# Kernel tuning notes

Hardware: AMD Instinct MI355X
Metric: run time of the kernel (lower is better)

The kernel has to match this reference:

```python
import jax, jax.numpy as jnp
import numpy as np

B, S, D = 2, 2048, 1024
H = 16
HD = D // H  # 64


def setup_inputs() -> dict:
    key = jax.random.key(0)
    k = jax.random.split(key, 6)
    s = 0.02
    return {
        "x": jax.random.normal(k[0], (B, S, D), dtype=jnp.float32),
        "wq": jax.random.normal(k[1], (D, D), dtype=jnp.float32) * s,
        "wk": jax.random.normal(k[2], (D, D), dtype=jnp.float32) * s,
        "wv": jax.random.normal(k[3], (D, D), dtype=jnp.float32) * s,
        "wo": jax.random.normal(k[4], (D, D), dtype=jnp.float32) * s,
        "bo": jnp.zeros((D,), dtype=jnp.float32),
    }


def reference(x, wq, wk, wv, wo, bo):
    b, n, d = x.shape
    # nn.Linear: y = x @ W.T (qkv_bias=False)
    def proj(w):
        y = jnp.einsum('bnd,od->bno', x, w)
        return y.reshape(b, n, H, HD).transpose(0, 2, 1, 3)  # (b, H, n, hd)
    q, k, v = proj(wq), proj(wk), proj(wv)
    scores = jnp.einsum('bhqd,bhkd->bhqk', q, k) / jnp.sqrt(jnp.float32(HD))
    # NOTE: source code slices the causal mask but never applies it; softmax is unmasked.
    attn = jax.nn.softmax(scores, axis=-1)
    # dropout p=0.0 -> identity
    ctx = jnp.einsum('bhqk,bhkd->bhqd', attn, v)
    ctx = ctx.transpose(0, 2, 1, 3).reshape(b, n, d)
    return jnp.einsum('bnd,od->bno', ctx, wo) + bo
```

## Files before the change

kernel.cpp:

```cpp
#include <hip/hip_runtime.h>
#include <hip/hip_bf16.h>
#include <stdint.h>

typedef __attribute__((ext_vector_type(8))) short short8;
typedef __attribute__((ext_vector_type(4))) float float4v;
typedef __attribute__((ext_vector_type(4))) unsigned short ushort4v;

#define Bq 2
#define Sq 2048
#define Dq 1024
#define Hq 16
#define HDq 64

#define QSCALE 0.18033688011112042f

__device__ __forceinline__ unsigned short f2bf(float f) {
  union { float f; uint32_t u; } v; v.f = f;
  uint32_t r = (v.u + 0x7FFFu + ((v.u >> 16) & 1u)) >> 16;
  return (unsigned short)r;
}

__device__ __forceinline__ uint32_t pk2bf(float a, float b) {
  union { __hip_bfloat162 h; uint32_t u; } cv;
  cv.h = __float22bfloat162_rn(make_float2(a, b));
  return cv.u;
}

__device__ __forceinline__ void gl_lds16(const unsigned short* g, unsigned short* l) {
  __builtin_amdgcn_global_load_lds(
      (const __attribute__((address_space(1))) void*)g,
      (__attribute__((address_space(3))) void*)l, 16, 0, 0);
}

__global__ __launch_bounds__(256) void cvt_all_kernel(
    const float* __restrict__ x,
    const float* __restrict__ w0, const float* __restrict__ w1,
    const float* __restrict__ w2, const float* __restrict__ w3,
    unsigned short* __restrict__ xb, unsigned short* __restrict__ wb) {
  const int bid = blockIdx.x;
  const float* src;
  unsigned short* dst;
  int idx;
  if (bid < 4096) {
    src = x; dst = xb;
    idx = bid * 256 + threadIdx.x;
  } else {
    int j = (bid - 4096) * 256 + threadIdx.x;
    int z = j >> 18;
    src = (z == 0) ? w0 : (z == 1) ? w1 : (z == 2) ? w2 : w3;
    dst = wb + (size_t)z * 1048576;
    idx = j & 262143;
  }
  float4v f = ((const float4v*)src)[idx];
  ushort4v o;
#pragma unroll
  for (int q = 0; q < 4; q++) o[q] = f2bf(f[q]);
  ((ushort4v*)dst)[idx] = o;
}

template <bool OUTPROJ, int MT>
__global__ __launch_bounds__(256) void gemm_bt_kernel(
    const unsigned short* __restrict__ A,
    const unsigned short* __restrict__ W0,
    const unsigned short* __restrict__ W1,
    const unsigned short* __restrict__ W2,
    unsigned short* __restrict__ q_dst,
    unsigned short* __restrict__ k_dst,
    unsigned short* __restrict__ v_dst,
    float* __restrict__ f_dst,
    const float* __restrict__ bias) {
  constexpr int K = 1024;
  constexpr int NMB = MT / 32;
  constexpr int APASS = MT / 32;
  const int z = blockIdx.z;
  const unsigned short* W = (z == 0) ? W0 : (z == 1) ? W1 : W2;
  unsigned short* qkv = (z == 0) ? q_dst : (z == 1) ? k_dst : v_dst;

  __shared__ unsigned short Asm[MT * 64];
  __shared__ unsigned short Bsm[128 * 64];

  const int t = threadIdx.x;
  const int wave = t >> 6, lane = t & 63;
  const int quad = lane >> 4, l16 = lane & 15;
  const int wy = wave >> 1, wx = wave & 1;
  const int row0 = blockIdx.x * MT;
  const int col0 = blockIdx.y * 128;

  float4v zero = {0.f, 0.f, 0.f, 0.f};
  float4v acc[NMB][4];
#pragma unroll
  for (int i = 0; i < NMB; i++)
#pragma unroll
    for (int j = 0; j < 4; j++) acc[i][j] = zero;

  const int srow = t >> 3;
  const int sgl = ((t & 7) ^ (srow & 7)) << 3;
  const unsigned short* gA[APASS];
  const unsigned short* gB[4];
#pragma unroll
  for (int i = 0; i < APASS; i++)
    gA[i] = A + (size_t)(row0 + i * 32 + srow) * K + sgl;
#pragma unroll
  for (int i = 0; i < 4; i++)
    gB[i] = W + (size_t)(col0 + i * 32 + srow) * K + sgl;

  const int swl = (l16 & 7);

  for (int k0 = 0; k0 < K; k0 += 64) {
#pragma unroll
    for (int i = 0; i < APASS; i++) gl_lds16(gA[i] + k0, &Asm[i * 2048 + t * 8]);
#pragma unroll
    for (int i = 0; i < 4; i++) gl_lds16(gB[i] + k0, &Bsm[i * 2048 + t * 8]);
    __syncthreads();
    short8 af[NMB][2], bf[4][2];
#pragma unroll
    for (int ks = 0; ks < 2; ks++) {
#pragma unroll
      for (int mb = 0; mb < NMB; mb++) {
        int row = wy * (MT / 2) + mb * 16 + l16;
        int pg = (ks * 4 + quad) ^ swl;
        af[mb][ks] = *(const short8*)(&Asm[row * 64 + pg * 8]);
      }
#pragma unroll
      for (int nb = 0; nb < 4; nb++) {
        int row = wx * 64 + nb * 16 + l16;
        int pg = (ks * 4 + quad) ^ swl;
        bf[nb][ks] = *(const short8*)(&Bsm[row * 64 + pg * 8]);
      }
    }
#pragma unroll
    for (int ks = 0; ks < 2; ks++)
#pragma unroll
      for (int mb = 0; mb < NMB; mb++)
#pragma unroll
        for (int nb = 0; nb < 4; nb++)
          acc[mb][nb] = __builtin_amdgcn_mfma_f32_16x16x32_bf16(af[mb][ks], bf[nb][ks], acc[mb][nb], 0, 0, 0);
    __syncthreads();
  }

  const float qsc = (!OUTPROJ && z == 0) ? QSCALE : 1.0f;
#pragma unroll
  for (int mb = 0; mb < NMB; mb++) {
#pragma unroll
    for (int nb = 0; nb < 4; nb++) {
#pragma unroll
      for (int r = 0; r < 4; r++) {
        int row = row0 + wy * (MT / 2) + mb * 16 + quad * 4 + r;
        int o = col0 + wx * 64 + nb * 16 + l16;
        float val = acc[mb][nb][r];
        if (OUTPROJ) {
          f_dst[(size_t)row * 1024 + o] = val + bias[o];
        } else {
          int b = row >> 11, s = row & 2047;
          int h = o >> 6, hd = o & 63;
          qkv[(size_t)((b * Hq + h) * Sq + s) * HDq + hd] = f2bf(val * qsc);
        }
      }
    }
  }
}

__global__ __launch_bounds__(256) void attn_kernel(
    const unsigned short* __restrict__ Q,
    const unsigned short* __restrict__ Kg,
    const unsigned short* __restrict__ Vg,
    unsigned short* __restrict__ ctx) {
  constexpr int KSTR = 68;
  constexpr int VSTR = 136;
  const int bh = blockIdx.y;
  const int q0 = blockIdx.x * 128;
  const int t = threadIdx.x;
  const int wave = t >> 6, lane = t & 63;
  const int quad = lane >> 4, l16 = lane & 15;

  __shared__ unsigned short Ksm[128 * KSTR];
  __shared__ unsigned short Vsm[64 * VSTR];

  const unsigned short* Qb = Q + (size_t)bh * Sq * HDq;
  const unsigned short* Kb = Kg + (size_t)bh * Sq * HDq;
  const unsigned short* Vb = Vg + (size_t)bh * Sq * HDq;

  short8 qf[2][2];
#pragma unroll
  for (int rb = 0; rb < 2; rb++)
#pragma unroll
    for (int ks = 0; ks < 2; ks++)
      qf[rb][ks] = *(const short8*)(Qb + (size_t)(q0 + wave * 32 + rb * 16 + l16) * HDq + ks * 32 + quad * 8);

  short8 ones;
#pragma unroll
  for (int j = 0; j < 8; j++) ones[j] = (short)0x3F80;

  float4v zero = {0.f, 0.f, 0.f, 0.f};
  float4v of[2][4];
  float4v dsum[2] = {zero, zero};
#pragma unroll
  for (int rb = 0; rb < 2; rb++)
#pragma unroll
    for (int hb = 0; hb < 4; hb++) of[rb][hb] = zero;

  const int kr0 = t >> 3, kc = (t & 7) << 3;
  const int vr2 = (t & 63) * 2;
  const int vc8 = (t >> 6) << 3;
  const int sig = (vr2 & ~31) + (((vr2 >> 2) & 3) << 3) + (((vr2 >> 4) & 1) << 2) + (vr2 & 3);

  short8 kpr[4], vpr0[2], vpr1[2];
#pragma unroll
  for (int i = 0; i < 4; i++)
    kpr[i] = *(const short8*)(Kb + (size_t)(kr0 + i * 32) * HDq + kc);
#pragma unroll
  for (int i = 0; i < 2; i++) {
    vpr0[i] = *(const short8*)(Vb + (size_t)vr2 * HDq + vc8 + i * 32);
    vpr1[i] = *(const short8*)(Vb + (size_t)(vr2 + 1) * HDq + vc8 + i * 32);
  }

  for (int kt = 0; kt < Sq; kt += 128) {
#pragma unroll
    for (int i = 0; i < 4; i++)
      *(short8*)(&Ksm[(kr0 + i * 32) * KSTR + kc]) = kpr[i];
#pragma unroll
    for (int i = 0; i < 2; i++)
#pragma unroll
      for (int j = 0; j < 8; j++) {
        uint32_t pk = (uint32_t)(unsigned short)vpr0[i][j] |
                      ((uint32_t)(unsigned short)vpr1[i][j] << 16);
        *(uint32_t*)(&Vsm[(vc8 + i * 32 + j) * VSTR + sig]) = pk;
      }
    __syncthreads();

    if (kt + 128 < Sq) {
      const unsigned short* Kn = Kb + (size_t)(kt + 128) * HDq;
      const unsigned short* Vn = Vb + (size_t)(kt + 128) * HDq;
#pragma unroll
      for (int i = 0; i < 4; i++)
        kpr[i] = *(const short8*)(Kn + (size_t)(kr0 + i * 32) * HDq + kc);
#pragma unroll
      for (int i = 0; i < 2; i++) {
        vpr0[i] = *(const short8*)(Vn + (size_t)vr2 * HDq + vc8 + i * 32);
        vpr1[i] = *(const short8*)(Vn + (size_t)(vr2 + 1) * HDq + vc8 + i * 32);
      }
    }

#pragma unroll
    for (int p = 0; p < 4; p++) {
      float4v sf[2][2];
#pragma unroll
      for (int rb = 0; rb < 2; rb++)
#pragma unroll
        for (int s = 0; s < 2; s++) sf[rb][s] = zero;
#pragma unroll
      for (int s = 0; s < 2; s++)
#pragma unroll
        for (int ks = 0; ks < 2; ks++) {
          short8 kf = *(const short8*)(&Ksm[(p * 32 + s * 16 + l16) * KSTR + ks * 32 + quad * 8]);
#pragma unroll
          for (int rb = 0; rb < 2; rb++)
            sf[rb][s] = __builtin_amdgcn_mfma_f32_16x16x32_bf16(kf, qf[rb][ks], sf[rb][s], 0, 0, 0);
        }
      short8 pf[2];
#pragma unroll
      for (int rb = 0; rb < 2; rb++) {
        union { uint32_t u[4]; short8 v; } pw;
#pragma unroll
        for (int s = 0; s < 2; s++)
#pragma unroll
          for (int rp = 0; rp < 2; rp++) {
            float pa = __builtin_amdgcn_exp2f(sf[rb][s][rp * 2]);
            float pb = __builtin_amdgcn_exp2f(sf[rb][s][rp * 2 + 1]);
            pw.u[s * 2 + rp] = pk2bf(pa, pb);
          }
        pf[rb] = pw.v;
      }
#pragma unroll
      for (int rb = 0; rb < 2; rb++)
        dsum[rb] = __builtin_amdgcn_mfma_f32_16x16x32_bf16(pf[rb], ones, dsum[rb], 0, 0, 0);
#pragma unroll
      for (int hb = 0; hb < 4; hb++) {
        short8 vf = *(const short8*)(&Vsm[(hb * 16 + l16) * VSTR + p * 32 + quad * 8]);
#pragma unroll
        for (int rb = 0; rb < 2; rb++)
          of[rb][hb] = __builtin_amdgcn_mfma_f32_16x16x32_bf16(pf[rb], vf, of[rb][hb], 0, 0, 0);
      }
    }
    __syncthreads();
  }

  const int b = bh >> 4, h = bh & 15;
#pragma unroll
  for (int rb = 0; rb < 2; rb++) {
    float4v dinv;
#pragma unroll
    for (int r = 0; r < 4; r++) dinv[r] = 1.0f / dsum[rb][r];
#pragma unroll
    for (int hb = 0; hb < 4; hb++)
#pragma unroll
      for (int r = 0; r < 4; r++) {
        int srow = q0 + wave * 32 + rb * 16 + quad * 4 + r;
        int d = h * 64 + hb * 16 + l16;
        ctx[(size_t)(b * Sq + srow) * Dq + d] = f2bf(of[rb][hb][r] * dinv[r]);
      }
  }
}

extern "C" void kernel_launch(void* const* d_in, const int* in_sizes, int n_in,
                              void* d_out, int out_size, void* d_ws, size_t ws_size,
                              hipStream_t stream) {
  (void)in_sizes; (void)n_in; (void)out_size; (void)ws_size;
  const float* x  = (const float*)d_in[0];
  const float* wq = (const float*)d_in[1];
  const float* wk = (const float*)d_in[2];
  const float* wv = (const float*)d_in[3];
  const float* wo = (const float*)d_in[4];
  const float* bo = (const float*)d_in[5];
  float* out = (float*)d_out;

  char* ws = (char*)d_ws;
  const size_t MB = 1u << 20;
  unsigned short* xb  = (unsigned short*)(ws + 0 * MB);
  unsigned short* wqb = (unsigned short*)(ws + 8 * MB);
  unsigned short* wkb = (unsigned short*)(ws + 10 * MB);
  unsigned short* wvb = (unsigned short*)(ws + 12 * MB);
  unsigned short* wob = (unsigned short*)(ws + 14 * MB);
  unsigned short* qb  = (unsigned short*)(ws + 16 * MB);
  unsigned short* kb  = (unsigned short*)(ws + 24 * MB);
  unsigned short* vb  = (unsigned short*)(ws + 32 * MB);
  unsigned short* cxb = (unsigned short*)(ws + 40 * MB);

  cvt_all_kernel<<<8192, 256, 0, stream>>>(x, wq, wk, wv, wo, xb, wqb);

  gemm_bt_kernel<false, 128><<<dim3(32, 8, 3), 256, 0, stream>>>(
      xb, wqb, wkb, wvb, qb, kb, vb, nullptr, nullptr);
  attn_kernel<<<dim3(16, 32), 256, 0, stream>>>(qb, kb, vb, cxb);
  gemm_bt_kernel<true, 64><<<dim3(64, 8, 1), 256, 0, stream>>>(
      cxb, wob, wob, wob, nullptr, nullptr, nullptr, out, bo);
}
```

Measured before the change: 187.1 us.

## Split attention block across eight waves with sixteen query rows each

The attention kernel now runs 512 threads per block. Each of eight waves owns 16 query rows instead of four waves owning 32 rows each, and the K/V staging loads are redistributed over the larger thread count. This cuts per-wave register use and doubles the waves available to hide MFMA and exp latency. In exchange, each K and V fragment read from LDS now feeds half as many MFMAs, roughly doubling shared-memory read traffic per useful operation.

Result: no change. 185.6 us (-0.8%).

```diff
diff --git a/kernel.cpp b/kernel.cpp
--- a/kernel.cpp
+++ b/kernel.cpp
@@ -160,7 +160,7 @@
   }
 }
 
-__global__ __launch_bounds__(256) void attn_kernel(
+__global__ __launch_bounds__(512) void attn_kernel(
     const unsigned short* __restrict__ Q,
     const unsigned short* __restrict__ Kg,
     const unsigned short* __restrict__ Vg,
@@ -180,126 +180,97 @@
   const unsigned short* Kb = Kg + (size_t)bh * Sq * HDq;
   const unsigned short* Vb = Vg + (size_t)bh * Sq * HDq;
 
-  short8 qf[2][2];
-#pragma unroll
-  for (int rb = 0; rb < 2; rb++)
-#pragma unroll
-    for (int ks = 0; ks < 2; ks++)
-      qf[rb][ks] = *(const short8*)(Qb + (size_t)(q0 + wave * 32 + rb * 16 + l16) * HDq + ks * 32 + quad * 8);
+  short8 qf[2];
+#pragma unroll
+  for (int ks = 0; ks < 2; ks++)
+    qf[ks] = *(const short8*)(Qb + (size_t)(q0 + wave * 16 + l16) * HDq + ks * 32 + quad * 8);
 
   short8 ones;
 #pragma unroll
   for (int j = 0; j < 8; j++) ones[j] = (short)0x3F80;
 
   float4v zero = {0.f, 0.f, 0.f, 0.f};
-  float4v of[2][4];
-  float4v dsum[2] = {zero, zero};
-#pragma unroll
-  for (int rb = 0; rb < 2; rb++)
-#pragma unroll
-    for (int hb = 0; hb < 4; hb++) of[rb][hb] = zero;
+  float4v of[4];
+  float4v dsum = zero;
+#pragma unroll
+  for (int hb = 0; hb < 4; hb++) of[hb] = zero;
 
   const int kr0 = t >> 3, kc = (t & 7) << 3;
   const int vr2 = (t & 63) * 2;
   const int vc8 = (t >> 6) << 3;
   const int sig = (vr2 & ~31) + (((vr2 >> 2) & 3) << 3) + (((vr2 >> 4) & 1) << 2) + (vr2 & 3);
 
-  short8 kpr[4], vpr0[2], vpr1[2];
-#pragma unroll
-  for (int i = 0; i < 4; i++)
-    kpr[i] = *(const short8*)(Kb + (size_t)(kr0 + i * 32) * HDq + kc);
-#pragma unroll
-  for (int i = 0; i < 2; i++) {
-    vpr0[i] = *(const short8*)(Vb + (size_t)vr2 * HDq + vc8 + i * 32);
-    vpr1[i] = *(const short8*)(Vb + (size_t)(vr2 + 1) * HDq + vc8 + i * 32);
-  }
+  short8 kpr[2], vpr0, vpr1;
+#pragma unroll
+  for (int i = 0; i < 2; i++)
+    kpr[i] = *(const short8*)(Kb + (size_t)(kr0 + i * 64) * HDq + kc);
+  vpr0 = *(const short8*)(Vb + (size_t)vr2 * HDq + vc8);
+  vpr1 = *(const short8*)(Vb + (size_t)(vr2 + 1) * HDq + vc8);
 
   for (int kt = 0; kt < Sq; kt += 128) {
 #pragma unroll
-    for (int i = 0; i < 4; i++)
-      *(short8*)(&Ksm[(kr0 + i * 32) * KSTR + kc]) = kpr[i];
-#pragma unroll
     for (int i = 0; i < 2; i++)
-#pragma unroll
-      for (int j = 0; j < 8; j++) {
-        uint32_t pk = (uint32_t)(unsigned short)vpr0[i][j] |
-                      ((uint32_t)(unsigned short)vpr1[i][j] << 16);
-        *(uint32_t*)(&Vsm[(vc8 + i * 32 + j) * VSTR + sig]) = pk;
-      }
+      *(short8*)(&Ksm[(kr0 + i * 64) * KSTR + kc]) = kpr[i];
+#pragma unroll
+    for (int j = 0; j < 8; j++) {
+      uint32_t pk = (uint32_t)(unsigned short)vpr0[j] |
+                    ((uint32_t)(unsigned short)vpr1[j] << 16);
+      *(uint32_t*)(&Vsm[(vc8 + j) * VSTR + sig]) = pk;
+    }
     __syncthreads();
 
     if (kt + 128 < Sq) {
       const unsigned short* Kn = Kb + (size_t)(kt + 128) * HDq;
       const unsigned short* Vn = Vb + (size_t)(kt + 128) * HDq;
 #pragma unroll
-      for (int i = 0; i < 4; i++)
-        kpr[i] = *(const short8*)(Kn + (size_t)(kr0 + i * 32) * HDq + kc);
-#pragma unroll
-      for (int i = 0; i < 2; i++) {
-        vpr0[i] = *(const short8*)(Vn + (size_t)vr2 * HDq + vc8 + i * 32);
-        vpr1[i] = *(const short8*)(Vn + (size_t)(vr2 + 1) * HDq + vc8 + i * 32);
-      }
+      for (int i = 0; i < 2; i++)
+        kpr[i] = *(const short8*)(Kn + (size_t)(kr0 + i * 64) * HDq + kc);
+      vpr0 = *(const short8*)(Vn + (size_t)vr2 * HDq + vc8);
+      vpr1 = *(const short8*)(Vn + (size_t)(vr2 + 1) * HDq + vc8);
     }
 
 #pragma unroll
     for (int p = 0; p < 4; p++) {
-      float4v sf[2][2];
-#pragma unroll
-      for (int rb = 0; rb < 2; rb++)
-#pragma unroll
-        for (int s = 0; s < 2; s++) sf[rb][s] = zero;
+      float4v sf[2] = {zero, zero};
 #pragma unroll
       for (int s = 0; s < 2; s++)
 #pragma unroll
         for (int ks = 0; ks < 2; ks++) {
           short8 kf = *(const short8*)(&Ksm[(p * 32 + s * 16 + l16) * KSTR + ks * 32 + quad * 8]);
-#pragma unroll
-          for (int rb = 0; rb < 2; rb++)
-            sf[rb][s] = __builtin_amdgcn_mfma_f32_16x16x32_bf16(kf, qf[rb][ks], sf[rb][s], 0, 0, 0);
+          sf[s] = __builtin_amdgcn_mfma_f32_16x16x32_bf16(kf, qf[ks], sf[s], 0, 0, 0);
         }
-      short8 pf[2];
-#pragma unroll
-      for (int rb = 0; rb < 2; rb++) {
-        union { uint32_t u[4]; short8 v; } pw;
-#pragma unroll
-        for (int s = 0; s < 2; s++)
-#pragma unroll
-          for (int rp = 0; rp < 2; rp++) {
-            float pa = __builtin_amdgcn_exp2f(sf[rb][s][rp * 2]);
-            float pb = __builtin_amdgcn_exp2f(sf[rb][s][rp * 2 + 1]);
-            pw.u[s * 2 + rp] = pk2bf(pa, pb);
-          }
-        pf[rb] = pw.v;
-      }
-#pragma unroll
-      for (int rb = 0; rb < 2; rb++)
-        dsum[rb] = __builtin_amdgcn_mfma_f32_16x16x32_bf16(pf[rb], ones, dsum[rb], 0, 0, 0);
+      union { uint32_t u[4]; short8 v; } pw;
+#pragma unroll
+      for (int s = 0; s < 2; s++)
+#pragma unroll
+        for (int rp = 0; rp < 2; rp++) {
+          float pa = __builtin_amdgcn_exp2f(sf[s][rp * 2]);
+          float pb = __builtin_amdgcn_exp2f(sf[s][rp * 2 + 1]);
+          pw.u[s * 2 + rp] = pk2bf(pa, pb);
+        }
+      short8 pf = pw.v;
+      dsum = __builtin_amdgcn_mfma_f32_16x16x32_bf16(pf, ones, dsum, 0, 0, 0);
 #pragma unroll
       for (int hb = 0; hb < 4; hb++) {
         short8 vf = *(const short8*)(&Vsm[(hb * 16 + l16) * VSTR + p * 32 + quad * 8]);
-#pragma unroll
-        for (int rb = 0; rb < 2; rb++)
-          of[rb][hb] = __builtin_amdgcn_mfma_f32_16x16x32_bf16(pf[rb], vf, of[rb][hb], 0, 0, 0);
+        of[hb] = __builtin_amdgcn_mfma_f32_16x16x32_bf16(pf, vf, of[hb], 0, 0, 0);
       }
     }
     __syncthreads();
   }
 
   const int b = bh >> 4, h = bh & 15;
-#pragma unroll
-  for (int rb = 0; rb < 2; rb++) {
-    float4v dinv;
-#pragma unroll
-    for (int r = 0; r < 4; r++) dinv[r] = 1.0f / dsum[rb][r];
-#pragma unroll
-    for (int hb = 0; hb < 4; hb++)
-#pragma unroll
-      for (int r = 0; r < 4; r++) {
-        int srow = q0 + wave * 32 + rb * 16 + quad * 4 + r;
-        int d = h * 64 + hb * 16 + l16;
-        ctx[(size_t)(b * Sq + srow) * Dq + d] = f2bf(of[rb][hb][r] * dinv[r]);
-      }
-  }
+  float4v dinv;
+#pragma unroll
+  for (int r = 0; r < 4; r++) dinv[r] = 1.0f / dsum[r];
+#pragma unroll
+  for (int hb = 0; hb < 4; hb++)
+#pragma unroll
+    for (int r = 0; r < 4; r++) {
+      int srow = q0 + wave * 16 + quad * 4 + r;
+      int d = h * 64 + hb * 16 + l16;
+      ctx[(size_t)(b * Sq + srow) * Dq + d] = f2bf(of[hb][r] * dinv[r]);
+    }
 }
 
 extern "C" void kernel_launch(void* const* d_in, const int* in_sizes, int n_in,
@@ -330,7 +301,7 @@
 
   gemm_bt_kernel<false, 128><<<dim3(32, 8, 3), 256, 0, stream>>>(
       xb, wqb, wkb, wvb, qb, kb, vb, nullptr, nullptr);
-  attn_kernel<<<dim3(16, 32), 256, 0, stream>>>(qb, kb, vb, cxb);
+  attn_kernel<<<dim3(16, 32), 512, 0, stream>>>(qb, kb, vb, cxb);
   gemm_bt_kernel<true, 64><<<dim3(64, 8, 1), 256, 0, stream>>>(
       cxb, wob, wob, wob, nullptr, nullptr, nullptr, out, bo);
 }
```
